# Kernel tuning notes

Hardware: AMD Instinct MI355X
Metric: run time of the kernel (lower is better)

The kernel has to match this reference:

```python
import jax, jax.numpy as jnp
import numpy as np

K, NC, NA = 9, 13, 5
NB, NH, NW = 128, 26, 26
NT, L = 50, 2 * K + 3
NOOBJ, OBJ, SIL = 1.0, 5.0, 0.6
COORD_S, CLASS_S = 1.0, 1.0
PRETRAIN_EPOCHS = 15
TH, SHARP = 80.0, 2.0                      # corner-conf distance threshold (px), sharpness
SCALE = np.array([640.0, 480.0], np.float32)  # im_width, im_height used by corner_confidences
CONF0 = float(np.exp(SHARP) - 1.0)
ANCHORS = np.array([1.482, 2.2412, 2.0501, 3.1265, 2.3946, 4.6891,
                    3.1018, 3.991, 3.4879, 5.8851], np.float32).reshape(NA, 2)


def setup_inputs():
    k1, k2 = jax.random.split(jax.random.key(0))
    output = jax.random.normal(k1, (NB, NA * (2 * K + 1 + NC), NH, NW), dtype=jnp.float32)
    target = jax.random.uniform(k2, (NB, NT * L), dtype=jnp.float32)
    return {"output": output, "target": target, "epoch": 20}


def _corner_conf(pred, gt):
    # pred, gt: [..., K, 2] normalized corners -> mean per-corner confidence [...]
    d = jnp.sqrt((((pred - gt) * jnp.asarray(SCALE)) ** 2).sum(-1))  # pixel distance [..., K]
    c = (jnp.exp(SHARP * (1.0 - d / TH)) - 1.0) / CONF0
    return jnp.where(d < TH, c, 0.0).mean(-1)


def _region_loss(output, target, epoch):
    nAnch, nPix = NA * NH * NW, NH * NW
    tgt = jax.lax.stop_gradient(target).reshape(NB, NT, L)
    out = output.reshape(NB, NA, 2 * K + 1 + NC, NH, NW)
    # keypoint 0 gets sigmoid, the rest are raw offsets
    xs = jnp.concatenate([jax.nn.sigmoid(out[:, :, 0:1]), out[:, :, 2:2 * K:2]], axis=2)  # [B,A,K,H,W]
    ys = jnp.concatenate([jax.nn.sigmoid(out[:, :, 1:2]), out[:, :, 3:2 * K:2]], axis=2)
    conf = jax.nn.sigmoid(out[:, :, 2 * K])                             # [B,A,H,W]
    cls_logits = jnp.transpose(out[:, :, 2 * K + 1:], (0, 1, 3, 4, 2))  # [B,A,H,W,NC]

    gxg = jnp.arange(NW, dtype=jnp.float32)
    gyg = jnp.arange(NH, dtype=jnp.float32)
    px = (jax.lax.stop_gradient(xs) + gxg) / NW            # detached, as torch uses .data
    py = (jax.lax.stop_gradient(ys) + gyg[:, None]) / NH
    # pred corners per anchor cell, flat anchor index = a*H*W + j*W + i -> [B, A*H*W, K, 2]
    pc = jnp.transpose(jnp.stack([px, py], -1), (0, 1, 3, 4, 2, 5)).reshape(NB, nAnch, K, 2)

    gt_xy = tgt[:, :, 1:1 + 2 * K].reshape(NB, NT, K, 2)
    # torch loop breaks at first target with x1 == 0 -> cumulative validity
    valid = jnp.cumprod((tgt[:, :, 1] != 0).astype(jnp.int32), axis=1) > 0  # [B,T]

    # pass 1: max corner confidence over valid GT, per anchor cell
    def max_conf_step(cur, inp):
        gt_t, v_t = inp                                    # [B,K,2], [B]
        c = _corner_conf(pc, gt_t[:, None]).reshape(NB, NA, NH, NW)
        return jnp.where(v_t[:, None, None, None], jnp.maximum(cur, c), cur), None

    cur_confs, _ = jax.lax.scan(max_conf_step, jnp.zeros((NB, NA, NH, NW), jnp.float32),
                                (jnp.swapaxes(gt_xy, 0, 1), valid.T))
    conf_mask0 = jnp.where(cur_confs > SIL, 0.0, NOOBJ)

    # per-target quantities (vectorized over b,t)
    gx = gt_xy[..., 0] * NW                                # [B,T,K]
    gy = gt_xy[..., 1] * NH
    gi0 = jnp.clip(jnp.floor(gx[:, :, 0]).astype(jnp.int32), 0, NW - 1)  # [B,T]
    gj0 = jnp.clip(jnp.floor(gy[:, :, 0]).astype(jnp.int32), 0, NH - 1)
    # pred_box is fetched with best_n == -1 (as in the source); emulate torch negative flat index via mod
    flat_idx = jnp.mod(jnp.arange(NB)[:, None] * nAnch - nPix + gj0 * NW + gi0, NB * nAnch)
    pred_box = pc.reshape(NB * nAnch, K, 2)[flat_idx]      # [B,T,K,2]
    conf_t = _corner_conf(pred_box, gt_xy)                 # [B,T]
    gw = tgt[:, :, L - 2] * NW
    gh = tgt[:, :, L - 1] * NH
    aw, ah = ANCHORS[:, 0], ANCHORS[:, 1]
    mw = jnp.minimum(aw, gw[..., None])                    # centered-box IoU (bbox_iou, cxcywh)
    mh = jnp.minimum(ah, gh[..., None])
    inter = mw * mh
    iou = inter / (aw * ah + (gw * gh)[..., None] - inter)
    best_n = jnp.argmax(iou, axis=-1).astype(jnp.int32)    # [B,T] (first max, like strict '>')
    txv = gx - gi0[..., None].astype(jnp.float32)          # [B,T,K]
    tyv = gy - gj0[..., None].astype(jnp.float32)
    tclsv = tgt[:, :, 0]

    # pass 2: sequential scatter matching torch overwrite order over t
    barange = jnp.arange(NB)
    z = jnp.zeros((NB, NA, NH, NW), jnp.float32)
    zk = jnp.zeros((NB, NA, NH, NW, K), jnp.float32)

    def scatter_step(carry, inp):
        cm, clm, cfm, tx, ty, tcf, tcl = carry
        v, bn, gj, gi, cft, txt, tyt, tct = inp
        idx = (barange, bn, gj, gi)
        vk = v[:, None]
        cm = cm.at[idx].set(jnp.where(v, 1.0, cm[idx]))
        clm = clm.at[idx].set(jnp.where(v, 1.0, clm[idx]))
        cfm = cfm.at[idx].set(jnp.where(v, OBJ, cfm[idx]))
        tx = tx.at[idx].set(jnp.where(vk, txt, tx[idx]))
        ty = ty.at[idx].set(jnp.where(vk, tyt, ty[idx]))
        tcf = tcf.at[idx].set(jnp.where(v, cft, tcf[idx]))
        tcl = tcl.at[idx].set(jnp.where(v, tct, tcl[idx]))
        return (cm, clm, cfm, tx, ty, tcf, tcl), None

    inps = (valid.T, best_n.T, gj0.T, gi0.T, conf_t.T,
            jnp.swapaxes(txv, 0, 1), jnp.swapaxes(tyv, 0, 1), tclsv.T)
    (coord_mask, cls_mask, conf_mask, tx, ty, tconf, tcls), _ = jax.lax.scan(
        scatter_step, (z, z, conf_mask0, zk, zk, z, z), inps)

    # losses
    xsT = jnp.transpose(xs, (0, 1, 3, 4, 2))               # [B,A,H,W,K]
    ysT = jnp.transpose(ys, (0, 1, 3, 4, 2))
    cmk = coord_mask[..., None]
    loss_x = 0.5 * COORD_S * jnp.sum(((xsT - tx) * cmk) ** 2)
    loss_y = 0.5 * COORD_S * jnp.sum(((ysT - ty) * cmk) ** 2)
    sq = jnp.sqrt(conf_mask)
    loss_conf = 0.5 * jnp.sum(((conf - tconf) * sq) ** 2)
    labels = jnp.clip(tcls.astype(jnp.int32), 0, NC - 1)
    ce = -jnp.take_along_axis(jax.nn.log_softmax(cls_logits, axis=-1),
                              labels[..., None], axis=-1)[..., 0]
    loss_cls = CLASS_S * jnp.sum(ce * cls_mask)
    loss = loss_x + loss_y + loss_cls
    if epoch > PRETRAIN_EPOCHS:
        loss = loss + loss_conf
    return loss


def reference(output, target, epoch):
    return _region_loss(output, target, epoch)
```

## Files before the change

### kernel.cpp

```cpp
#include <hip/hip_runtime.h>
#include <math.h>

#define KK     9
#define NCLS   13
#define NANC   5
#define NBB    128
#define NHH    26
#define NWW    26
#define NTT    50
#define LL     21
#define CHC    32
#define NPIX   676
#define NANCHT 3380
#define NCELLT 432640

#define LOG2E_F   1.4426950408889634f
#define K1C       2.8853900817779268f
#define K2C       0.036067376022224085f
#define SXW       24.615384615384617f
#define SYH       18.461538461538463f
#define THRESH_S  43.500902934225507f
#define CULL_T2   292.0f
#define CONF_T_SCALE 0.017390849194407297f
#define OBJ_W     5.0f
#define EPOCH_PRETRAIN 15

typedef __attribute__((ext_vector_type(2))) float f2;

static __device__ __forceinline__ float fast_exp2(float x){
#if __has_builtin(__builtin_amdgcn_exp2f)
  return __builtin_amdgcn_exp2f(x);
#else
  return exp2f(x);
#endif
}
static __device__ __forceinline__ float fast_sqrt(float x){
#if __has_builtin(__builtin_amdgcn_sqrtf)
  return __builtin_amdgcn_sqrtf(x);
#else
  return sqrtf(x);
#endif
}
static __device__ __forceinline__ float sigmoidf_(float x){
  return 1.0f/(1.0f + fast_exp2(-LOG2E_F*x));
}

__constant__ float c_anch[10] = {1.482f,2.2412f,2.0501f,3.1265f,2.3946f,4.6891f,
                                 3.1018f,3.991f,3.4879f,5.8851f};


__global__ __launch_bounds__(64) void prep_kernel(const float* __restrict__ tgt,
                                                  float* __restrict__ gts_neg,
                                                  int* __restrict__ nvalid){
  int b = blockIdx.x;
  int t = threadIdx.x;
  const float* trow = tgt + (size_t)b*NTT*LL;
  float v1 = (t < NTT) ? trow[t*LL + 1] : 0.0f;
  unsigned long long mk = __ballot(t < NTT && v1 != 0.0f);
  int firstInvalid = __ffsll(~mk) - 1;
  if (t == 0) nvalid[b] = firstInvalid;
  for (int idx = t; idx < NTT*2*KK; idx += 64){
    int tt = idx / (2*KK);
    int c  = idx - tt*(2*KK);
    float v = trow[tt*LL + 1 + c];
    float s = (c & 1) ? 480.0f : 640.0f;
    gts_neg[((size_t)b*NTT + tt)*(2*KK) + c] = -(v * s);
  }
}

__global__ __launch_bounds__(256) void region_confmask_kernel(
    const float* __restrict__ outp, const float* __restrict__ gts_neg,
    const int* __restrict__ nvalid, unsigned char* __restrict__ mask,
    double* __restrict__ partials){
  int b = blockIdx.y;
  int cell = blockIdx.x * blockDim.x + threadIdx.x;
  float contrib = 0.0f;
  if (cell < NANCHT){
    int a   = cell / NPIX;
    int rem = cell - a*NPIX;
    int j   = rem / NWW;
    int i   = rem - j*NWW;
    const float* base = outp + (((size_t)b*NANC + a)*CHC)*NPIX + rem;

    f2 P[KK];
#pragma unroll
    for (int k = 0; k < KK; ++k){
      float rx = base[(2*k)*NPIX];
      float ry = base[(2*k+1)*NPIX];
      if (k == 0){ rx = sigmoidf_(rx); ry = sigmoidf_(ry); }
      P[k].x = (rx + (float)i) * SXW;
      P[k].y = (ry + (float)j) * SYH;
    }

    int nv = nvalid[b];
    const float* g = gts_neg + (size_t)b*NTT*(2*KK);
    unsigned long long qbits = 0ull;
    for (int t = 0; t < nv; ++t, g += 2*KK){
      float m = 1e30f;
#pragma unroll
      for (int k = 0; k < KK; ++k){
        f2 gv; gv.x = g[2*k]; gv.y = g[2*k+1];
        f2 d  = P[k] + gv;
        f2 sq = d * d;
        m = fminf(m, sq.x + sq.y);
      }
      if (m < CULL_T2) qbits |= (1ull << t);
    }

    int m0 = 1;
    if (__any(qbits != 0ull)){
      bool exc = false;
      while (qbits){
        int t = __ffsll((long long)qbits) - 1;
        qbits &= qbits - 1;
        const float* gg = gts_neg + ((size_t)b*NTT + t)*(2*KK);
        float s = 0.0f;
#pragma unroll
        for (int k = 0; k < KK; ++k){
          float dx = P[k].x + gg[2*k];
          float dy = P[k].y + gg[2*k+1];
          float d  = fast_sqrt(fmaf(dy, dy, dx*dx));
          float e  = fast_exp2(fmaf(d, -K2C, K1C));
          s += fmaxf(e, 1.0f);
        }
        exc |= (s > THRESH_S);
      }
      if (exc) m0 = 0;
    }
    mask[(size_t)b*NANCHT + cell] = (unsigned char)m0;
    float cf = sigmoidf_(base[(2*KK)*NPIX]);
    contrib = m0 ? 0.5f*cf*cf : 0.0f;
  }
#pragma unroll
  for (int o = 32; o > 0; o >>= 1) contrib += __shfl_xor(contrib, o, 64);
  __shared__ float wsum[4];
  int wid = threadIdx.x >> 6, lane = threadIdx.x & 63;
  if (lane == 0) wsum[wid] = contrib;
  __syncthreads();
  if (threadIdx.x == 0){
    double tot = (double)wsum[0] + (double)wsum[1] + (double)wsum[2] + (double)wsum[3];
    partials[blockIdx.y * gridDim.x + blockIdx.x] = tot;
  }
}

__global__ __launch_bounds__(64) void scatter_loss_kernel(
    const float* __restrict__ outp, const float* __restrict__ tgt,
    const int* __restrict__ nvalid, const unsigned char* __restrict__ mask,
    double* __restrict__ bc_part){
  int b = blockIdx.x;
  int t = threadIdx.x;
  __shared__ int keys[NTT];
  int nv = nvalid[b];
  bool valid = (t < nv);

  int key = -1, gi0 = 0, gj0 = 0, bn = 0;
  float txv[KK], tyv[KK];
  float conf_t = 0.0f, tcls = 0.0f;

  if (t < NTT){
    const float* trow = tgt + ((size_t)b*NTT + t)*LL;
    tcls = trow[0];
    float gx0 = trow[1]*(float)NWW;
    float gy0 = trow[2]*(float)NHH;
    gi0 = min(max((int)floorf(gx0), 0), NWW-1);
    gj0 = min(max((int)floorf(gy0), 0), NHH-1);
#pragma unroll
    for (int k = 0; k < KK; ++k){
      txv[k] = trow[1+2*k]*(float)NWW - (float)gi0;
      tyv[k] = trow[2+2*k]*(float)NHH - (float)gj0;
    }
    float gw = trow[LL-2]*(float)NWW, gh = trow[LL-1]*(float)NHH;
    float best = -1.0f;
    for (int a = 0; a < NANC; ++a){
      float aw = c_anch[2*a], ah = c_anch[2*a+1];
      float inter = fminf(aw, gw) * fminf(ah, gh);
      float iou = inter / (aw*ah + gw*gh - inter);
      if (iou > best){ best = iou; bn = a; }
    }
    key = bn*NPIX + gj0*NWW + gi0;
    keys[t] = key;

    long f = (long)b*NANCHT - NPIX + gj0*NWW + gi0;
    if (f < 0) f += NCELLT;
    int bb  = (int)(f / NANCHT);
    int rr  = (int)(f - (long)bb*NANCHT);
    int aa  = rr / NPIX;
    int rr2 = rr - aa*NPIX;
    int jj  = rr2 / NWW;
    int ii  = rr2 - jj*NWW;
    const float* pbase = outp + (((size_t)bb*NANC + aa)*CHC)*NPIX + rr2;
    float s = 0.0f;
#pragma unroll
    for (int k = 0; k < KK; ++k){
      float rx = pbase[(2*k)*NPIX], ry = pbase[(2*k+1)*NPIX];
      if (k == 0){ rx = sigmoidf_(rx); ry = sigmoidf_(ry); }
      float Pxx = (rx + (float)ii)*SXW, Pyy = (ry + (float)jj)*SYH;
      float dx = Pxx - trow[1+2*k]*640.0f;
      float dy = Pyy - trow[2+2*k]*480.0f;
      float d  = fast_sqrt(fmaf(dy, dy, dx*dx));
      float e  = fast_exp2(fmaf(d, -K2C, K1C));
      s += fmaxf(e, 1.0f);
    }
    conf_t = (s - 9.0f) * CONF_T_SCALE;
  }
  __syncthreads();

  bool winner = valid;
  if (valid){
    for (int u = t+1; u < nv; ++u) if (keys[u] == key){ winner = false; break; }
  }

  double lx = 0.0, ly = 0.0, lcls = 0.0, lcf = 0.0;
  if (winner){
    const float* cbase = outp + (((size_t)b*NANC + bn)*CHC)*NPIX + gj0*NWW + gi0;
    float sx = 0.0f, sy = 0.0f;
#pragma unroll
    for (int k = 0; k < KK; ++k){
      float rx = cbase[(2*k)*NPIX], ry = cbase[(2*k+1)*NPIX];
      if (k == 0){ rx = sigmoidf_(rx); ry = sigmoidf_(ry); }
      float dx = rx - txv[k], dy = ry - tyv[k];
      sx = fmaf(dx, dx, sx); sy = fmaf(dy, dy, sy);
    }
    lx = 0.5*(double)sx; ly = 0.5*(double)sy;

    float lg[NCLS], mx = -1e30f;
#pragma unroll
    for (int c = 0; c < NCLS; ++c){ lg[c] = cbase[(2*KK+1+c)*NPIX]; mx = fmaxf(mx, lg[c]); }
    float se = 0.0f;
#pragma unroll
    for (int c = 0; c < NCLS; ++c) se += fast_exp2((lg[c]-mx)*LOG2E_F);
    int label = min(max((int)tcls, 0), NCLS-1);
    lcls = (double)(mx + logf(se) - lg[label]);

    float cf = sigmoidf_(cbase[(2*KK)*NPIX]);
    int m0 = mask[(size_t)b*NANCHT + (size_t)bn*NPIX + gj0*NWW + gi0];
    float dcf = cf - conf_t;
    lcf = 0.5*OBJ_W*(double)(dcf*dcf) - (m0 ? 0.5*(double)(cf*cf) : 0.0);
  }

#pragma unroll
  for (int o = 32; o > 0; o >>= 1){
    lx  += __shfl_xor(lx,  o, 64);
    ly  += __shfl_xor(ly,  o, 64);
    lcls+= __shfl_xor(lcls,o, 64);
    lcf += __shfl_xor(lcf, o, 64);
  }
  if (threadIdx.x == 0){
    double* bp = bc_part + (size_t)b*4;
    bp[0] = lx; bp[1] = ly; bp[2] = lcls; bp[3] = lcf;
  }
}

__global__ __launch_bounds__(256) void finalize_kernel(
    const double* __restrict__ bc_part, const double* __restrict__ partials,
    const int* __restrict__ epoch_p, float* __restrict__ outv){
  int tid = threadIdx.x;
  double vx=0, vy=0, vc=0, vf=0, vb=0;
  for (int i = tid; i < NBB; i += 256){
    vx += bc_part[4*i]; vy += bc_part[4*i+1];
    vc += bc_part[4*i+2]; vf += bc_part[4*i+3];
  }
  for (int i = tid; i < 14*NBB; i += 256) vb += partials[i];
#pragma unroll
  for (int o = 32; o > 0; o >>= 1){
    vx += __shfl_xor(vx, o, 64); vy += __shfl_xor(vy, o, 64);
    vc += __shfl_xor(vc, o, 64); vf += __shfl_xor(vf, o, 64);
    vb += __shfl_xor(vb, o, 64);
  }
  __shared__ double sm[5][4];
  int wid = tid >> 6, lane = tid & 63;
  if (lane == 0){ sm[0][wid]=vx; sm[1][wid]=vy; sm[2][wid]=vc; sm[3][wid]=vf; sm[4][wid]=vb; }
  __syncthreads();
  if (tid == 0){
    double fx=0, fy=0, fc=0, ff=0, fb=0;
    for (int w = 0; w < 4; ++w){ fx+=sm[0][w]; fy+=sm[1][w]; fc+=sm[2][w]; ff+=sm[3][w]; fb+=sm[4][w]; }
    double loss = fx + fy + fc;
    if (*epoch_p > EPOCH_PRETRAIN) loss += ff + fb;
    outv[0] = (float)loss;
  }
}

extern "C" void kernel_launch(void* const* d_in, const int* in_sizes, int n_in,
                              void* d_out, int out_size, void* d_ws, size_t ws_size,
                              hipStream_t stream){
  (void)in_sizes; (void)n_in; (void)out_size; (void)ws_size;
  const float* outp = (const float*)d_in[0];
  const float* tgt  = (const float*)d_in[1];
  const int*   ep   = (const int*)d_in[2];
  float* outv = (float*)d_out;
  char* ws = (char*)d_ws;

  double* bc_part  = (double*)(ws);
  double* partials = (double*)(ws + 4096);
  float*  gts_neg  = (float*) (ws + 18432);
  int*    nvalid   = (int*)   (ws + 479232);
  unsigned char* mask = (unsigned char*)(ws + 479744);

  prep_kernel<<<dim3(NBB), dim3(64), 0, stream>>>(tgt, gts_neg, nvalid);
  region_confmask_kernel<<<dim3(14, NBB), dim3(256), 0, stream>>>(outp, gts_neg, nvalid, mask, partials);
  scatter_loss_kernel<<<dim3(NBB), dim3(64), 0, stream>>>(outp, tgt, nvalid, mask, bc_part);
  finalize_kernel<<<dim3(1), dim3(256), 0, stream>>>(bc_part, partials, ep, outv);
}
```

Before: 142.6 us.

## Stage GT corners in LDS with split x/y layout and pack mask as bits

The prep kernel now writes ground-truth corners in a planar x/y layout, padded to 20 floats per target with a large sentinel in the pad slots. The main kernel copies the whole per-batch table into shared memory once per block. The culling loop now handles corner pairs with packed two-wide FMA/min, and the per-anchor mask is written as ballot bitwords instead of bytes. This removes repeated global/scalar loads in the inner target loop and cuts mask traffic, at the cost of an LDS fill and a barrier per block.

```diff
diff --git a/kernel.cpp b/kernel.cpp
--- a/kernel.cpp
+++ b/kernel.cpp
@@ -13,6 +13,8 @@
 #define NPIX   676
 #define NANCHT 3380
 #define NCELLT 432640
+#define GTS    20
+#define MWPB   106
 
 #define LOG2E_F   1.4426950408889634f
 #define K1C       2.8853900817779268f
@@ -24,22 +26,15 @@
 #define CONF_T_SCALE 0.017390849194407297f
 #define OBJ_W     5.0f
 #define EPOCH_PRETRAIN 15
+#define BIGV      6.0e18f
 
 typedef __attribute__((ext_vector_type(2))) float f2;
 
 static __device__ __forceinline__ float fast_exp2(float x){
-#if __has_builtin(__builtin_amdgcn_exp2f)
   return __builtin_amdgcn_exp2f(x);
-#else
-  return exp2f(x);
-#endif
 }
 static __device__ __forceinline__ float fast_sqrt(float x){
-#if __has_builtin(__builtin_amdgcn_sqrtf)
   return __builtin_amdgcn_sqrtf(x);
-#else
-  return sqrtf(x);
-#endif
 }
 static __device__ __forceinline__ float sigmoidf_(float x){
   return 1.0f/(1.0f + fast_exp2(-LOG2E_F*x));
@@ -59,21 +54,30 @@
   unsigned long long mk = __ballot(t < NTT && v1 != 0.0f);
   int firstInvalid = __ffsll(~mk) - 1;
   if (t == 0) nvalid[b] = firstInvalid;
-  for (int idx = t; idx < NTT*2*KK; idx += 64){
-    int tt = idx / (2*KK);
-    int c  = idx - tt*(2*KK);
-    float v = trow[tt*LL + 1 + c];
-    float s = (c & 1) ? 480.0f : 640.0f;
-    gts_neg[((size_t)b*NTT + tt)*(2*KK) + c] = -(v * s);
+  for (int idx = t; idx < NTT*GTS; idx += 64){
+    int tt = idx / GTS;
+    int c  = idx - tt*GTS;
+    float v;
+    if (c == 9 || c == 19)      v = BIGV;
+    else if (c < 9)             v = -(trow[tt*LL + 1 + 2*c] * 640.0f);
+    else                        v = -(trow[tt*LL + 2 + 2*(c-10)] * 480.0f);
+    gts_neg[(size_t)b*NTT*GTS + idx] = v;
   }
 }
 
 __global__ __launch_bounds__(256) void region_confmask_kernel(
     const float* __restrict__ outp, const float* __restrict__ gts_neg,
-    const int* __restrict__ nvalid, unsigned char* __restrict__ mask,
+    const int* __restrict__ nvalid, unsigned int* __restrict__ maskw,
     double* __restrict__ partials){
   int b = blockIdx.y;
   int cell = blockIdx.x * blockDim.x + threadIdx.x;
+
+  __shared__ float sgt[NTT*GTS] __attribute__((aligned(16)));
+  for (int idx = threadIdx.x; idx < NTT*GTS; idx += 256)
+    sgt[idx] = gts_neg[(size_t)b*NTT*GTS + idx];
+  __syncthreads();
+
+  int m0 = 1;
   float contrib = 0.0f;
   if (cell < NANCHT){
     int a   = cell / NPIX;
@@ -82,43 +86,45 @@
     int i   = rem - j*NWW;
     const float* base = outp + (((size_t)b*NANC + a)*CHC)*NPIX + rem;
 
-    f2 P[KK];
+    f2 Pxp[5], Pyp[5];
 #pragma unroll
     for (int k = 0; k < KK; ++k){
       float rx = base[(2*k)*NPIX];
       float ry = base[(2*k+1)*NPIX];
       if (k == 0){ rx = sigmoidf_(rx); ry = sigmoidf_(ry); }
-      P[k].x = (rx + (float)i) * SXW;
-      P[k].y = (ry + (float)j) * SYH;
-    }
+      Pxp[k>>1][k&1] = (rx + (float)i) * SXW;
+      Pyp[k>>1][k&1] = (ry + (float)j) * SYH;
+    }
+    Pxp[4][1] = 0.0f; Pyp[4][1] = 0.0f;
 
     int nv = nvalid[b];
-    const float* g = gts_neg + (size_t)b*NTT*(2*KK);
     unsigned long long qbits = 0ull;
-    for (int t = 0; t < nv; ++t, g += 2*KK){
-      float m = 1e30f;
-#pragma unroll
-      for (int k = 0; k < KK; ++k){
-        f2 gv; gv.x = g[2*k]; gv.y = g[2*k+1];
-        f2 d  = P[k] + gv;
-        f2 sq = d * d;
-        m = fminf(m, sq.x + sq.y);
+#pragma unroll 2
+    for (int t = 0; t < nv; ++t){
+      const f2* gx = (const f2*)(sgt + t*GTS);
+      const f2* gy = gx + 5;
+      f2 m2 = {1e30f, 1e30f};
+#pragma unroll
+      for (int p = 0; p < 5; ++p){
+        f2 dx = Pxp[p] + gx[p];
+        f2 dy = Pyp[p] + gy[p];
+        f2 r  = __builtin_elementwise_fma(dy, dy, dx*dx);
+        m2 = __builtin_elementwise_min(m2, r);
       }
-      if (m < CULL_T2) qbits |= (1ull << t);
-    }
-
-    int m0 = 1;
+      if (fminf(m2.x, m2.y) < CULL_T2) qbits |= (1ull << t);
+    }
+
     if (__any(qbits != 0ull)){
       bool exc = false;
       while (qbits){
         int t = __ffsll((long long)qbits) - 1;
         qbits &= qbits - 1;
-        const float* gg = gts_neg + ((size_t)b*NTT + t)*(2*KK);
+        const float* gg = sgt + t*GTS;
         float s = 0.0f;
 #pragma unroll
         for (int k = 0; k < KK; ++k){
-          float dx = P[k].x + gg[2*k];
-          float dy = P[k].y + gg[2*k+1];
+          float dx = Pxp[k>>1][k&1] + gg[k];
+          float dy = Pyp[k>>1][k&1] + gg[10+k];
           float d  = fast_sqrt(fmaf(dy, dy, dx*dx));
           float e  = fast_exp2(fmaf(d, -K2C, K1C));
           s += fmaxf(e, 1.0f);
@@ -127,14 +133,22 @@
       }
       if (exc) m0 = 0;
     }
-    mask[(size_t)b*NANCHT + cell] = (unsigned char)m0;
     float cf = sigmoidf_(base[(2*KK)*NPIX]);
     contrib = m0 ? 0.5f*cf*cf : 0.0f;
   }
+
+  unsigned long long mb = __ballot(m0 != 0);
+  int lane = threadIdx.x & 63;
+  int wavebase = blockIdx.x * 256 + (threadIdx.x & ~63);
+  if ((lane & 31) == 0 && wavebase < NANCHT){
+    unsigned int w = (lane == 0) ? (unsigned int)mb : (unsigned int)(mb >> 32);
+    maskw[(size_t)b*MWPB + (wavebase >> 5) + (lane >> 5)] = w;
+  }
+
 #pragma unroll
   for (int o = 32; o > 0; o >>= 1) contrib += __shfl_xor(contrib, o, 64);
   __shared__ float wsum[4];
-  int wid = threadIdx.x >> 6, lane = threadIdx.x & 63;
+  int wid = threadIdx.x >> 6;
   if (lane == 0) wsum[wid] = contrib;
   __syncthreads();
   if (threadIdx.x == 0){
@@ -145,7 +159,7 @@
 
 __global__ __launch_bounds__(64) void scatter_loss_kernel(
     const float* __restrict__ outp, const float* __restrict__ tgt,
-    const int* __restrict__ nvalid, const unsigned char* __restrict__ mask,
+    const int* __restrict__ nvalid, const unsigned int* __restrict__ maskw,
     double* __restrict__ bc_part){
   int b = blockIdx.x;
   int t = threadIdx.x;
@@ -233,7 +247,8 @@
     lcls = (double)(mx + logf(se) - lg[label]);
 
     float cf = sigmoidf_(cbase[(2*KK)*NPIX]);
-    int m0 = mask[(size_t)b*NANCHT + (size_t)bn*NPIX + gj0*NWW + gi0];
+    int idx = bn*NPIX + gj0*NWW + gi0;
+    int m0 = (maskw[(size_t)b*MWPB + (idx >> 5)] >> (idx & 31)) & 1;
     float dcf = cf - conf_t;
     lcf = 0.5*OBJ_W*(double)(dcf*dcf) - (m0 ? 0.5*(double)(cf*cf) : 0.0);
   }
@@ -293,11 +308,11 @@
   double* bc_part  = (double*)(ws);
   double* partials = (double*)(ws + 4096);
   float*  gts_neg  = (float*) (ws + 18432);
-  int*    nvalid   = (int*)   (ws + 479232);
-  unsigned char* mask = (unsigned char*)(ws + 479744);
+  int*    nvalid   = (int*)   (ws + 530432);
+  unsigned int* maskw = (unsigned int*)(ws + 530944);
 
   prep_kernel<<<dim3(NBB), dim3(64), 0, stream>>>(tgt, gts_neg, nvalid);
-  region_confmask_kernel<<<dim3(14, NBB), dim3(256), 0, stream>>>(outp, gts_neg, nvalid, mask, partials);
-  scatter_loss_kernel<<<dim3(NBB), dim3(64), 0, stream>>>(outp, tgt, nvalid, mask, bc_part);
+  region_confmask_kernel<<<dim3(14, NBB), dim3(256), 0, stream>>>(outp, gts_neg, nvalid, maskw, partials);
+  scatter_loss_kernel<<<dim3(NBB), dim3(64), 0, stream>>>(outp, tgt, nvalid, maskw, bc_part);
   finalize_kernel<<<dim3(1), dim3(256), 0, stream>>>(bc_part, partials, ep, outv);
 }
```

Result: faster. 135.5 us (-4.9%).
